# Kernel optimization log

Measured on AMD Instinct MI355X. Metric: run time of the kernel, lower is better.

## Reference

```python
import jax, jax.numpy as jnp
import numpy as np

N, B, L = 1000, 16, 12
H, IN_DIM, OUT_DIM, E = 64, 3, 1, 16000


def _gru_cell(x, h, Wi, Wh, bi, bh):
    # torch nn.GRU gate order: r, z, n
    gi = x @ Wi.T + bi
    gh = h @ Wh.T + bh
    ir, iz, inn = jnp.split(gi, 3, axis=-1)
    hr, hz, hn = jnp.split(gh, 3, axis=-1)
    r = jax.nn.sigmoid(ir + hr)
    z = jax.nn.sigmoid(iz + hz)
    n = jnp.tanh(inn + r * hn)
    return (1.0 - z) * n + z * h


def setup_inputs():
    key = jax.random.key(0)
    ks = jax.random.split(key, 24)
    def rn(k, shape, s=0.1):
        return jax.random.normal(k, shape, dtype=jnp.float32) * s
    return {
        "hidden0": rn(ks[0], (N, B, H), 1.0),
        "hidden1": rn(ks[1], (N, B, H), 1.0),
        "features": rn(ks[2], (N, H), 1.0),
        "labels": rn(ks[3], (N, B, L, IN_DIM), 1.0),
        "edge_index": jax.random.randint(ks[4], (2, E), 0, N),
        # GRU1: input_dim -> H
        "Wi1": rn(ks[5], (3 * H, IN_DIM)), "Wh1": rn(ks[6], (3 * H, H)),
        "bi1": rn(ks[7], (3 * H,)), "bh1": rn(ks[8], (3 * H,)),
        # MetaGAT MLP: 2H -> 16 -> 2 -> 2H*H
        "W1": rn(ks[9], (16, 2 * H)), "b1": rn(ks[10], (16,)),
        "W2": rn(ks[11], (2, 16)), "b2": rn(ks[12], (2,)),
        "W3": rn(ks[13], (2 * H * H, 2)), "b3": rn(ks[14], (2 * H * H,)),
        # GRU2: H -> H
        "Wi2": rn(ks[15], (3 * H, H)), "Wh2": rn(ks[16], (3 * H, H)),
        "bi2": rn(ks[17], (3 * H,)), "bh2": rn(ks[18], (3 * H,)),
        # output layer: 2H -> OUT_DIM
        "Wo": rn(ks[19], (OUT_DIM, 2 * H)), "bo": rn(ks[20], (OUT_DIM,)),
    }


def reference(hidden0, hidden1, features, labels, edge_index,
              Wi1, Wh1, bi1, bh1, W1, b1, W2, b2, W3, b3,
              Wi2, Wh2, bi2, bh2, Wo, bo):
    n, b, length, _ = labels.shape
    h = Wh1.shape[1]
    out_dim = Wo.shape[0]
    in_dim = Wi1.shape[1]
    aux = labels[..., out_dim:]  # [N,B,L,aux_dim]
    # add self loops (as in MetaGAT.forward)
    loops = jnp.arange(n)
    src = jnp.concatenate([edge_index[0], loops])  # j, source
    dst = jnp.concatenate([edge_index[1], loops])  # i, target
    # per-edge weight matrices; features are constant across timesteps so hoist
    ft = jnp.concatenate([features[dst], features[src]], axis=-1)  # [Etot,2H]
    w = jax.nn.sigmoid(ft @ W1.T + b1)
    w = jax.nn.sigmoid(w @ W2.T + b2)
    w = (w @ W3.T + b3).reshape(-1, 2 * h, h)  # [Etot,2H,H]
    feat_b = jnp.broadcast_to(features[:, None, :], (n, b, features.shape[-1]))

    def step(carry, idx):
        h0, h1, prev = carry
        aux_prev = jnp.take(aux, jnp.maximum(idx - 1, 0), axis=2)  # [N,B,aux]
        # eval path (train_mode=False): feed back previous prediction
        data = jnp.where(idx == 0,
                         jnp.zeros((n, b, in_dim), labels.dtype),
                         jnp.concatenate([prev, aux_prev], axis=-1))
        h0n = _gru_cell(data.reshape(n * b, in_dim), h0.reshape(n * b, h),
                        Wi1, Wh1, bi1, bh1).reshape(n, b, h)
        # MetaGAT message passing
        st_j = h0n[src]                                  # [Etot,B,H]
        st = jnp.concatenate([h0n[dst], st_j], axis=-1)  # [Etot,B,2H]
        alpha = jax.nn.leaky_relu(jnp.einsum('ebk,ekh->ebh', st, w), 0.01)
        alpha = jax.nn.softmax(alpha, axis=1)            # softmax over batch dim (faithful to source)
        agg = jax.ops.segment_sum(alpha * st_j, dst, num_segments=n)
        gat = jax.nn.relu(agg)                           # [N,B,H]
        h1n = _gru_cell(gat.reshape(n * b, h), h1.reshape(n * b, h),
                        Wi2, Wh2, bi2, bh2).reshape(n, b, h)
        pred = jnp.concatenate([h1n, feat_b], axis=-1) @ Wo.T + bo  # [N,B,out_dim]
        return (h0n, h1n, pred), pred

    init = (hidden0, hidden1, jnp.zeros((n, b, out_dim), labels.dtype))
    _, preds = jax.lax.scan(step, init, jnp.arange(length))
    return jnp.moveaxis(preds, 0, 2)  # [N,B,L,out_dim]
```

## Files before the change

### kernel.cpp

```cpp
#include <hip/hip_runtime.h>

#define N_NODES 1000
#define BATCH 16
#define SEQ 12
#define IN_DIM 3
#define HDIM 64
#define E_EDGES 16000
#define EN (E_EDGES + N_NODES)
#define NB (N_NODES * BATCH)

typedef unsigned int u32;
typedef unsigned short u16;

__device__ __forceinline__ float sigmoidf(float x) { return 1.0f / (1.0f + expf(-x)); }

__device__ __forceinline__ u16 f2bf(float x) {
    u32 u = __builtin_bit_cast(u32, x);
    u32 r = (u + 0x7fffu + ((u >> 16) & 1u)) >> 16;
    return (u16)r;
}
__device__ __forceinline__ float bf2f(u32 h) {
    return __builtin_bit_cast(float, (h & 0xffffu) << 16);
}
__device__ __forceinline__ u32 pack2(float a, float b) {
    return (u32)f2bf(a) | ((u32)f2bf(b) << 16);
}

__global__ void prep_kernel(const float* __restrict__ hidden0,
                            const float* __restrict__ hidden1,
                            const float* __restrict__ features,
                            const float* __restrict__ W3,
                            const float* __restrict__ b3,
                            const float* __restrict__ Wo,
                            const float* __restrict__ bo,
                            const float* __restrict__ Wh1,
                            const float* __restrict__ Wi1,
                            const float* __restrict__ Wi2,
                            const float* __restrict__ Wh2,
                            float* __restrict__ h0, float* __restrict__ h1,
                            u32* __restrict__ WhPair,
                            u32* __restrict__ Mpair,
                            u32* __restrict__ W2pair,
                            float* __restrict__ Wi1T,
                            float* __restrict__ fpred)
{
    int tid = blockIdx.x * blockDim.x + threadIdx.x;
    int stride = gridDim.x * blockDim.x;

    for (int i = tid; i < NB * HDIM; i += stride) { h0[i] = hidden0[i]; h1[i] = hidden1[i]; }

    for (int i = tid; i < 32 * 192; i += stride) {
        int k2 = i / 192, rem = i % 192;
        int row = rem;
        WhPair[i] = pack2(Wh1[row * 64 + 2 * k2], Wh1[row * 64 + 2 * k2 + 1]);
    }

    for (int i = tid; i < 32 * 384; i += stride) {
        int k2 = i / 384, rem = i % 384;
        int c = rem / 64, h = rem % 64;
        int sel = c % 3;
        float v0, v1;
        {
            int k = 2 * k2;
            int kk = (c < 3 ? k : 64 + k) * 64 + h;
            v0 = (sel == 0) ? W3[kk * 2] : (sel == 1) ? W3[kk * 2 + 1] : b3[kk];
        }
        {
            int k = 2 * k2 + 1;
            int kk = (c < 3 ? k : 64 + k) * 64 + h;
            v1 = (sel == 0) ? W3[kk * 2] : (sel == 1) ? W3[kk * 2 + 1] : b3[kk];
        }
        Mpair[i] = pack2(v0, v1);
    }

    for (int i = tid; i < 32 * 384; i += stride) {
        int k2 = i / 384, rem = i % 384;
        int c = rem / 64, j = rem % 64;
        float v0, v1;
        if (c < 3) {
            int row = c * 64 + j;
            v0 = Wi2[row * 64 + 2 * k2]; v1 = Wi2[row * 64 + 2 * k2 + 1];
        } else {
            int row = (c - 3) * 64 + j;
            v0 = Wh2[row * 64 + 2 * k2]; v1 = Wh2[row * 64 + 2 * k2 + 1];
        }
        W2pair[i] = pack2(v0, v1);
    }

    for (int i = tid; i < 3 * 192; i += stride) {
        int c = i / 192, gj = i % 192;
        Wi1T[i] = Wi1[gj * 3 + c];
    }

    for (int n = tid; n < N_NODES; n += stride) {
        float acc = bo[0];
        for (int h = 0; h < HDIM; ++h) acc += features[n * HDIM + h] * Wo[64 + h];
        fpred[n] = acc;
    }
}

__global__ void deg_init_kernel(int* __restrict__ deg)
{
    int n = blockIdx.x * blockDim.x + threadIdx.x;
    if (n < N_NODES) deg[n] = 1;
}

__global__ void deg_count_kernel(const int* __restrict__ edge_index, int* __restrict__ deg)
{
    int e = blockIdx.x * blockDim.x + threadIdx.x;
    if (e < E_EDGES) atomicAdd(&deg[edge_index[E_EDGES + e]], 1);
}

__global__ __launch_bounds__(1024) void scan_kernel(const int* __restrict__ deg,
                                                    int* __restrict__ row_ptr,
                                                    int* __restrict__ row_fill)
{
    __shared__ int s[1024];
    int tid = threadIdx.x;
    int x = (tid < N_NODES) ? deg[tid] : 0;
    s[tid] = x;
    __syncthreads();
    for (int off = 1; off < 1024; off <<= 1) {
        int v = (tid >= off) ? s[tid - off] : 0;
        __syncthreads();
        s[tid] += v;
        __syncthreads();
    }
    int incl = s[tid];
    int excl = incl - x;
    if (tid < N_NODES) { row_ptr[tid] = excl; row_fill[tid] = excl; }
    if (tid == N_NODES - 1) row_ptr[N_NODES] = incl;
}

__global__ void scatter_kernel(const int* __restrict__ edge_index,
                               int* __restrict__ row_fill,
                               int* __restrict__ csr_src,
                               int* __restrict__ perm)
{
    int e = blockIdx.x * blockDim.x + threadIdx.x;
    if (e < E_EDGES) {
        int s = edge_index[e];
        int d = edge_index[E_EDGES + e];
        int p = atomicAdd(&row_fill[d], 1);
        csr_src[p] = s;
        perm[e] = p;
    } else if (e < EN) {
        int n = e - E_EDGES;
        int p = atomicAdd(&row_fill[n], 1);
        csr_src[p] = n;
        perm[e] = p;
    }
}

__global__ __launch_bounds__(256) void edge_mlp_kernel(const int* __restrict__ edge_index,
                                                       const float* __restrict__ features,
                                                       const float* __restrict__ W1,
                                                       const float* __restrict__ b1,
                                                       const float* __restrict__ W2,
                                                       const float* __restrict__ b2,
                                                       const int* __restrict__ perm,
                                                       float* __restrict__ csr_uv)
{
    int w = threadIdx.x >> 6, j = threadIdx.x & 63;
    int e = blockIdx.x * 4 + w;
    int s, d;
    if (e < E_EDGES) { s = edge_index[e]; d = edge_index[E_EDGES + e]; }
    else             { s = e - E_EDGES; d = s; }

    __shared__ float ft[4][128];
    __shared__ float w1s[4][16];
    ft[w][j]      = features[d * HDIM + j];
    ft[w][64 + j] = features[s * HDIM + j];
    __syncthreads();

    int o = j & 15, part = j >> 4;
    float acc = 0.0f;
    #pragma unroll 8
    for (int kk = 0; kk < 32; ++kk)
        acc += ft[w][part * 32 + kk] * W1[o * 128 + part * 32 + kk];
    acc += __shfl_xor(acc, 16, 64);
    acc += __shfl_xor(acc, 32, 64);
    if (j < 16) w1s[w][j] = sigmoidf(acc + b1[j]);
    __syncthreads();
    if (j < 2) {
        float a2 = b2[j];
        #pragma unroll
        for (int k = 0; k < 16; ++k) a2 += w1s[w][k] * W2[j * 16 + k];
        csr_uv[perm[e] * 2 + j] = sigmoidf(a2);
    }
}

__global__ __launch_bounds__(512) void gru1_proj_kernel(const float* __restrict__ labels,
                                                        const float* __restrict__ prev,
                                                        const float* __restrict__ Wi1T,
                                                        const u32* __restrict__ WhPair,
                                                        const float* __restrict__ bi1,
                                                        const float* __restrict__ bh1,
                                                        const u32* __restrict__ Mpair,
                                                        float* __restrict__ h0,
                                                        uint2* __restrict__ Pd,
                                                        uint2* __restrict__ Ps,
                                                        int t)
{
    int tid = threadIdx.x;
    int w = tid >> 6, j = tid & 63;
    int rbase = blockIdx.x * 64 + w * 8;

    __shared__ u32 sWh[32 * 192];
    __shared__ u32 sM[32 * 384];
    __shared__ float hs[64][64];

    for (int i = tid; i < 32 * 192; i += 512) sWh[i] = WhPair[i];
    for (int i = tid; i < 32 * 384; i += 512) sM[i] = Mpair[i];
    #pragma unroll
    for (int rr = 0; rr < 8; ++rr)
        hs[w * 8 + rr][j] = h0[(size_t)(rbase + rr) * HDIM + j];
    __syncthreads();

    float ar[8], az[8], an[8];
    {
        float br = bh1[j], bz = bh1[64 + j], bn = bh1[128 + j];
        #pragma unroll
        for (int rr = 0; rr < 8; ++rr) { ar[rr] = br; az[rr] = bz; an[rr] = bn; }
    }

    for (int k2 = 0; k2 < 32; ++k2) {
        u32 pr = sWh[k2 * 192 + j];
        u32 pz = sWh[k2 * 192 + 64 + j];
        u32 pn = sWh[k2 * 192 + 128 + j];
        float wr0 = bf2f(pr), wr1 = bf2f(pr >> 16);
        float wz0 = bf2f(pz), wz1 = bf2f(pz >> 16);
        float wn0 = bf2f(pn), wn1 = bf2f(pn >> 16);
        #pragma unroll
        for (int rr = 0; rr < 8; ++rr) {
            float2 h2 = *(const float2*)&hs[w * 8 + rr][2 * k2];
            ar[rr] = fmaf(wr0, h2.x, ar[rr]); ar[rr] = fmaf(wr1, h2.y, ar[rr]);
            az[rr] = fmaf(wz0, h2.x, az[rr]); az[rr] = fmaf(wz1, h2.y, az[rr]);
            an[rr] = fmaf(wn0, h2.x, an[rr]); an[rr] = fmaf(wn1, h2.y, an[rr]);
        }
    }

    float wi00 = Wi1T[j],       wi01 = Wi1T[64 + j],       wi02 = Wi1T[128 + j];
    float wi10 = Wi1T[192 + j], wi11 = Wi1T[192 + 64 + j], wi12 = Wi1T[192 + 128 + j];
    float wi20 = Wi1T[384 + j], wi21 = Wi1T[384 + 64 + j], wi22 = Wi1T[384 + 128 + j];
    float bir = bi1[j], biz = bi1[64 + j], bin_ = bi1[128 + j];

    #pragma unroll
    for (int rr = 0; rr < 8; ++rr) {
        int row = rbase + rr;
        float x0 = 0.f, x1 = 0.f, x2 = 0.f;
        if (t > 0) {
            x0 = prev[row];
            const float* lab = labels + ((size_t)row * SEQ + (t - 1)) * IN_DIM;
            x1 = lab[1]; x2 = lab[2];
        }
        float gir = bir  + x0 * wi00 + x1 * wi10 + x2 * wi20;
        float giz = biz  + x0 * wi01 + x1 * wi11 + x2 * wi21;
        float gin = bin_ + x0 * wi02 + x1 * wi12 + x2 * wi22;
        float rg = sigmoidf(gir + ar[rr]);
        float zg = sigmoidf(giz + az[rr]);
        float ng = tanhf(gin + rg * an[rr]);
        float hj = hs[w * 8 + rr][j];
        float hn = (1.0f - zg) * ng + zg * hj;
        h0[(size_t)row * HDIM + j] = hn;
        hs[w * 8 + rr][j] = hn;
    }

    float a0[8], a1[8], a2[8], a3[8], a4[8], a5[8];
    #pragma unroll
    for (int rr = 0; rr < 8; ++rr) { a0[rr]=0.f; a1[rr]=0.f; a2[rr]=0.f; a3[rr]=0.f; a4[rr]=0.f; a5[rr]=0.f; }

    for (int k2 = 0; k2 < 32; ++k2) {
        u32 p0 = sM[k2 * 384 + j];
        u32 p1 = sM[k2 * 384 + 64 + j];
        u32 p2 = sM[k2 * 384 + 128 + j];
        u32 p3 = sM[k2 * 384 + 192 + j];
        u32 p4 = sM[k2 * 384 + 256 + j];
        u32 p5 = sM[k2 * 384 + 320 + j];
        float m00 = bf2f(p0), m01 = bf2f(p0 >> 16);
        float m10 = bf2f(p1), m11 = bf2f(p1 >> 16);
        float m20 = bf2f(p2), m21 = bf2f(p2 >> 16);
        float m30 = bf2f(p3), m31 = bf2f(p3 >> 16);
        float m40 = bf2f(p4), m41 = bf2f(p4 >> 16);
        float m50 = bf2f(p5), m51 = bf2f(p5 >> 16);
        #pragma unroll
        for (int rr = 0; rr < 8; ++rr) {
            float2 h2 = *(const float2*)&hs[w * 8 + rr][2 * k2];
            a0[rr] = fmaf(m00, h2.x, a0[rr]); a0[rr] = fmaf(m01, h2.y, a0[rr]);
            a1[rr] = fmaf(m10, h2.x, a1[rr]); a1[rr] = fmaf(m11, h2.y, a1[rr]);
            a2[rr] = fmaf(m20, h2.x, a2[rr]); a2[rr] = fmaf(m21, h2.y, a2[rr]);
            a3[rr] = fmaf(m30, h2.x, a3[rr]); a3[rr] = fmaf(m31, h2.y, a3[rr]);
            a4[rr] = fmaf(m40, h2.x, a4[rr]); a4[rr] = fmaf(m41, h2.y, a4[rr]);
            a5[rr] = fmaf(m50, h2.x, a5[rr]); a5[rr] = fmaf(m51, h2.y, a5[rr]);
        }
    }

    #pragma unroll
    for (int rr = 0; rr < 8; ++rr) {
        size_t row = rbase + rr;
        float stj = hs[w * 8 + rr][j];
        Pd[row * 64 + j] = make_uint2(pack2(a0[rr], a1[rr]), pack2(a2[rr], 0.f));
        Ps[row * 64 + j] = make_uint2(pack2(a3[rr], a4[rr]), pack2(a5[rr], stj));
    }
}

__global__ __launch_bounds__(256) void edge_step_kernel(const int* __restrict__ row_ptr,
                                                        const int* __restrict__ csr_src,
                                                        const float* __restrict__ csr_uv,
                                                        const uint2* __restrict__ Pd,
                                                        const uint2* __restrict__ Ps,
                                                        float* __restrict__ agg)
{
    int d = blockIdx.x;
    int w = threadIdx.x >> 6, h = threadIdx.x & 63;

    uint2 pdreg[BATCH];
    #pragma unroll
    for (int b = 0; b < BATCH; ++b)
        pdreg[b] = Pd[((size_t)d * BATCH + b) * 64 + h];

    float acc[BATCH];
    #pragma unroll
    for (int b = 0; b < BATCH; ++b) acc[b] = 0.0f;

    int start = row_ptr[d], end = row_ptr[d + 1];
    for (int p = start + w; p < end; p += 4) {
        int s = csr_src[p];
        float u = csr_uv[p * 2], v = csr_uv[p * 2 + 1];

        float al[BATCH], stj[BATCH];
        #pragma unroll
        for (int b = 0; b < BATCH; ++b) {
            uint2 pd = pdreg[b];
            uint2 ps = Ps[((size_t)s * BATCH + b) * 64 + h];
            float a = u * (bf2f(pd.x) + bf2f(ps.x))
                    + v * (bf2f(pd.x >> 16) + bf2f(ps.x >> 16))
                    + bf2f(pd.y) + bf2f(ps.y);
            al[b] = (a > 0.0f) ? a : 0.01f * a;
            stj[b] = bf2f(ps.y >> 16);
        }
        float m = al[0];
        #pragma unroll
        for (int b = 1; b < BATCH; ++b) m = fmaxf(m, al[b]);
        float sum = 0.0f;
        #pragma unroll
        for (int b = 0; b < BATCH; ++b) { al[b] = expf(al[b] - m); sum += al[b]; }
        float inv = 1.0f / sum;
        #pragma unroll
        for (int b = 0; b < BATCH; ++b) acc[b] = fmaf(al[b] * inv, stj[b], acc[b]);
    }

    __shared__ float red[4][BATCH][HDIM];
    #pragma unroll
    for (int b = 0; b < BATCH; ++b) red[w][b][h] = acc[b];
    __syncthreads();

    for (int c = threadIdx.x; c < BATCH * HDIM; c += 256) {
        float s4 = red[0][0][c] + red[1][0][c] + red[2][0][c] + red[3][0][c];
        agg[(size_t)d * BATCH * HDIM + c] = s4;
    }
}

__global__ __launch_bounds__(512) void gru2_pred_kernel(const float* __restrict__ agg,
                                                        const u32* __restrict__ W2pair,
                                                        const float* __restrict__ bi2,
                                                        const float* __restrict__ bh2,
                                                        const float* __restrict__ Wo,
                                                        const float* __restrict__ fpred,
                                                        float* __restrict__ h1,
                                                        float* __restrict__ prev,
                                                        float* __restrict__ out,
                                                        int t)
{
    int tid = threadIdx.x;
    int w = tid >> 6, j = tid & 63;
    int rbase = blockIdx.x * 64 + w * 8;

    __shared__ u32 sW2[32 * 384];
    __shared__ float gs[64][64];
    __shared__ float hs[64][64];

    for (int i = tid; i < 32 * 384; i += 512) sW2[i] = W2pair[i];
    #pragma unroll
    for (int rr = 0; rr < 8; ++rr) {
        float g = agg[(size_t)(rbase + rr) * HDIM + j];
        gs[w * 8 + rr][j] = fmaxf(g, 0.0f);
        hs[w * 8 + rr][j] = h1[(size_t)(rbase + rr) * HDIM + j];
    }
    __syncthreads();

    float acr[8], acz[8], ain[8], ahn[8];
    {
        float b0 = bi2[j] + bh2[j], b1 = bi2[64 + j] + bh2[64 + j];
        float b2 = bi2[128 + j], c2 = bh2[128 + j];
        #pragma unroll
        for (int rr = 0; rr < 8; ++rr) { acr[rr] = b0; acz[rr] = b1; ain[rr] = b2; ahn[rr] = c2; }
    }

    for (int k2 = 0; k2 < 32; ++k2) {
        u32 pir = sW2[k2 * 384 + j];
        u32 piz = sW2[k2 * 384 + 64 + j];
        u32 pin = sW2[k2 * 384 + 128 + j];
        u32 phr = sW2[k2 * 384 + 192 + j];
        u32 phz = sW2[k2 * 384 + 256 + j];
        u32 phn = sW2[k2 * 384 + 320 + j];
        float wir0 = bf2f(pir), wir1 = bf2f(pir >> 16);
        float wiz0 = bf2f(piz), wiz1 = bf2f(piz >> 16);
        float win0 = bf2f(pin), win1 = bf2f(pin >> 16);
        float whr0 = bf2f(phr), whr1 = bf2f(phr >> 16);
        float whz0 = bf2f(phz), whz1 = bf2f(phz >> 16);
        float whn0 = bf2f(phn), whn1 = bf2f(phn >> 16);
        #pragma unroll
        for (int rr = 0; rr < 8; ++rr) {
            float2 g2 = *(const float2*)&gs[w * 8 + rr][2 * k2];
            float2 h2 = *(const float2*)&hs[w * 8 + rr][2 * k2];
            acr[rr] = fmaf(wir0, g2.x, acr[rr]); acr[rr] = fmaf(wir1, g2.y, acr[rr]);
            acr[rr] = fmaf(whr0, h2.x, acr[rr]); acr[rr] = fmaf(whr1, h2.y, acr[rr]);
            acz[rr] = fmaf(wiz0, g2.x, acz[rr]); acz[rr] = fmaf(wiz1, g2.y, acz[rr]);
            acz[rr] = fmaf(whz0, h2.x, acz[rr]); acz[rr] = fmaf(whz1, h2.y, acz[rr]);
            ain[rr] = fmaf(win0, g2.x, ain[rr]); ain[rr] = fmaf(win1, g2.y, ain[rr]);
            ahn[rr] = fmaf(whn0, h2.x, ahn[rr]); ahn[rr] = fmaf(whn1, h2.y, ahn[rr]);
        }
    }

    float woj = Wo[j];
    #pragma unroll
    for (int rr = 0; rr < 8; ++rr) {
        float rg = sigmoidf(acr[rr]);
        float zg = sigmoidf(acz[rr]);
        float ng = tanhf(ain[rr] + rg * ahn[rr]);
        float hj = hs[w * 8 + rr][j];
        float hn = (1.0f - zg) * ng + zg * hj;
        h1[(size_t)(rbase + rr) * HDIM + j] = hn;

        float part = hn * woj;
        #pragma unroll
        for (int off = 32; off; off >>= 1) part += __shfl_xor(part, off, 64);
        if (j == rr) {
            int row = rbase + rr;
            float p = part + fpred[row / BATCH];
            prev[row] = p;
            out[(size_t)row * SEQ + t] = p;
        }
    }
}

extern "C" void kernel_launch(void* const* d_in, const int* in_sizes, int n_in,
                              void* d_out, int out_size, void* d_ws, size_t ws_size,
                              hipStream_t stream)
{
    const float* hidden0  = (const float*)d_in[0];
    const float* hidden1  = (const float*)d_in[1];
    const float* features = (const float*)d_in[2];
    const float* labels   = (const float*)d_in[3];
    const int*   edge_idx = (const int*)d_in[4];
    const float* Wi1 = (const float*)d_in[5];
    const float* Wh1 = (const float*)d_in[6];
    const float* bi1 = (const float*)d_in[7];
    const float* bh1 = (const float*)d_in[8];
    const float* W1  = (const float*)d_in[9];
    const float* b1  = (const float*)d_in[10];
    const float* W2  = (const float*)d_in[11];
    const float* b2  = (const float*)d_in[12];
    const float* W3  = (const float*)d_in[13];
    const float* b3  = (const float*)d_in[14];
    const float* Wi2 = (const float*)d_in[15];
    const float* Wh2 = (const float*)d_in[16];
    const float* bi2 = (const float*)d_in[17];
    const float* bh2 = (const float*)d_in[18];
    const float* Wo  = (const float*)d_in[19];
    const float* bo  = (const float*)d_in[20];

    float* ws = (float*)d_ws;
    float* h0    = ws;  ws += NB * HDIM;
    float* h1    = ws;  ws += NB * HDIM;
    uint2* Pd    = (uint2*)ws;  ws += NB * HDIM * 2;
    uint2* Ps    = (uint2*)ws;  ws += NB * HDIM * 2;
    float* agg   = ws;  ws += NB * HDIM;
    float* csr_uv= ws;  ws += EN * 2;
    u32*   WhPair = (u32*)ws;  ws += 32 * 192;
    u32*   Mpair  = (u32*)ws;  ws += 32 * 384;
    u32*   W2pair = (u32*)ws;  ws += 32 * 384;
    float* Wi1T  = ws;  ws += 3 * 192;
    float* fpred = ws;  ws += N_NODES;
    float* prev  = ws;  ws += NB;
    int*   deg      = (int*)ws;  ws += N_NODES;
    int*   row_ptr  = (int*)ws;  ws += N_NODES + 1;
    int*   row_fill = (int*)ws;  ws += N_NODES;
    int*   csr_src  = (int*)ws;  ws += EN;
    int*   perm     = (int*)ws;  ws += EN;
    float* out   = (float*)d_out;

    prep_kernel<<<256, 256, 0, stream>>>(hidden0, hidden1, features, W3, b3, Wo, bo,
                                         Wh1, Wi1, Wi2, Wh2,
                                         h0, h1, WhPair, Mpair, W2pair, Wi1T, fpred);
    deg_init_kernel<<<(N_NODES + 255) / 256, 256, 0, stream>>>(deg);
    deg_count_kernel<<<(E_EDGES + 255) / 256, 256, 0, stream>>>(edge_idx, deg);
    scan_kernel<<<1, 1024, 0, stream>>>(deg, row_ptr, row_fill);
    scatter_kernel<<<(EN + 255) / 256, 256, 0, stream>>>(edge_idx, row_fill, csr_src, perm);
    edge_mlp_kernel<<<(EN + 3) / 4, 256, 0, stream>>>(edge_idx, features, W1, b1, W2, b2,
                                                      perm, csr_uv);

    for (int t = 0; t < SEQ; ++t) {
        gru1_proj_kernel<<<NB / 64, 512, 0, stream>>>(labels, prev, Wi1T, WhPair, bi1, bh1,
                                                      Mpair, h0, Pd, Ps, t);
        edge_step_kernel<<<N_NODES, 256, 0, stream>>>(row_ptr, csr_src, csr_uv, Pd, Ps, agg);
        gru2_pred_kernel<<<NB / 64, 512, 0, stream>>>(agg, W2pair, bi2, bh2, Wo, fpred,
                                                      h1, prev, out, t);
    }
}
```

Measured before the change: 1.045 ms.

## Replace per-timestep kernel triplet with a persistent cooperative kernel using grid sync

The 36 per-timestep launches are replaced by one cooperative kernel with one block per node. Each block keeps its node's GRU hidden states in shared memory across all timesteps and uses a grid-wide sync only before the edge aggregation. The source projections are double-buffered so the next step's writes never overwrite data another block is still reading. This removes launch overhead and global round-trips for h0, h1, Pd and agg, at the cost of grid-sync latency and a lower-occupancy fused kernel. The old path is kept as a fallback if the cooperative launch fails.

Result: slower. 2.606 ms (+149.3%).

```diff
diff --git a/kernel.cpp b/kernel.cpp
--- a/kernel.cpp
+++ b/kernel.cpp
@@ -1,4 +1,7 @@
 #include <hip/hip_runtime.h>
+#include <hip/hip_cooperative_groups.h>
+
+namespace cg = cooperative_groups;
 
 #define N_NODES 1000
 #define BATCH 16
@@ -50,8 +53,7 @@
     for (int i = tid; i < NB * HDIM; i += stride) { h0[i] = hidden0[i]; h1[i] = hidden1[i]; }
 
     for (int i = tid; i < 32 * 192; i += stride) {
-        int k2 = i / 192, rem = i % 192;
-        int row = rem;
+        int k2 = i / 192, row = i % 192;
         WhPair[i] = pack2(Wh1[row * 64 + 2 * k2], Wh1[row * 64 + 2 * k2 + 1]);
     }
 
@@ -187,6 +189,243 @@
         #pragma unroll
         for (int k = 0; k < 16; ++k) a2 += w1s[w][k] * W2[j * 16 + k];
         csr_uv[perm[e] * 2 + j] = sigmoidf(a2);
+    }
+}
+
+__global__ __launch_bounds__(256, 4) void persist_kernel(
+    const float* __restrict__ hidden0,
+    const float* __restrict__ hidden1,
+    const float* __restrict__ labels,
+    const int* __restrict__ row_ptr,
+    const int* __restrict__ csr_src,
+    const float* __restrict__ csr_uv,
+    const float* __restrict__ Wi1T,
+    const u32* __restrict__ WhPair,
+    const float* __restrict__ bi1,
+    const float* __restrict__ bh1,
+    const u32* __restrict__ Mpair,
+    const u32* __restrict__ W2pair,
+    const float* __restrict__ bi2,
+    const float* __restrict__ bh2,
+    const float* __restrict__ Wo,
+    const float* __restrict__ fpred,
+    uint2* __restrict__ PsA,
+    uint2* __restrict__ PsB,
+    float* __restrict__ out)
+{
+    cg::grid_group grid = cg::this_grid();
+
+    int d = blockIdx.x;
+    int tid = threadIdx.x;
+    int w = tid >> 6, j = tid & 63;
+    int rb = w * 4;
+    int growbase = d * BATCH;
+
+    __shared__ float hs0[BATCH][HDIM];
+    __shared__ float hs1[BATCH][HDIM];
+    __shared__ float gs[BATCH][HDIM];
+    __shared__ float red[4][BATCH][HDIM];
+    __shared__ uint2 sPd[BATCH][HDIM];
+    __shared__ float prevs[BATCH];
+
+    #pragma unroll
+    for (int rr = 0; rr < 4; ++rr) {
+        hs0[rb + rr][j] = hidden0[(size_t)(growbase + rb + rr) * HDIM + j];
+        hs1[rb + rr][j] = hidden1[(size_t)(growbase + rb + rr) * HDIM + j];
+    }
+    int start = row_ptr[d], end = row_ptr[d + 1];
+
+    for (int t = 0; t < SEQ; ++t) {
+        uint2* PsCur = (t & 1) ? PsB : PsA;
+
+        {
+            float bhr = bh1[j], bhz = bh1[64 + j], bhn = bh1[128 + j];
+            float ar[4], az[4], an[4];
+            #pragma unroll
+            for (int rr = 0; rr < 4; ++rr) { ar[rr] = bhr; az[rr] = bhz; an[rr] = bhn; }
+
+            for (int k2 = 0; k2 < 32; ++k2) {
+                u32 pr = WhPair[k2 * 192 + j];
+                u32 pz = WhPair[k2 * 192 + 64 + j];
+                u32 pn = WhPair[k2 * 192 + 128 + j];
+                float wr0 = bf2f(pr), wr1 = bf2f(pr >> 16);
+                float wz0 = bf2f(pz), wz1 = bf2f(pz >> 16);
+                float wn0 = bf2f(pn), wn1 = bf2f(pn >> 16);
+                #pragma unroll
+                for (int rr = 0; rr < 4; ++rr) {
+                    float2 h2 = *(const float2*)&hs0[rb + rr][2 * k2];
+                    ar[rr] = fmaf(wr0, h2.x, ar[rr]); ar[rr] = fmaf(wr1, h2.y, ar[rr]);
+                    az[rr] = fmaf(wz0, h2.x, az[rr]); az[rr] = fmaf(wz1, h2.y, az[rr]);
+                    an[rr] = fmaf(wn0, h2.x, an[rr]); an[rr] = fmaf(wn1, h2.y, an[rr]);
+                }
+            }
+
+            float wi00 = Wi1T[j],       wi01 = Wi1T[64 + j],       wi02 = Wi1T[128 + j];
+            float wi10 = Wi1T[192 + j], wi11 = Wi1T[192 + 64 + j], wi12 = Wi1T[192 + 128 + j];
+            float wi20 = Wi1T[384 + j], wi21 = Wi1T[384 + 64 + j], wi22 = Wi1T[384 + 128 + j];
+            float bir = bi1[j], biz = bi1[64 + j], bin_ = bi1[128 + j];
+
+            #pragma unroll
+            for (int rr = 0; rr < 4; ++rr) {
+                int lrow = rb + rr;
+                float x0 = 0.f, x1 = 0.f, x2 = 0.f;
+                if (t > 0) {
+                    x0 = prevs[lrow];
+                    const float* lab = labels + ((size_t)(growbase + lrow) * SEQ + (t - 1)) * IN_DIM;
+                    x1 = lab[1]; x2 = lab[2];
+                }
+                float gir = bir  + x0 * wi00 + x1 * wi10 + x2 * wi20;
+                float giz = biz  + x0 * wi01 + x1 * wi11 + x2 * wi21;
+                float gin = bin_ + x0 * wi02 + x1 * wi12 + x2 * wi22;
+                float rg = sigmoidf(gir + ar[rr]);
+                float zg = sigmoidf(giz + az[rr]);
+                float ng = tanhf(gin + rg * an[rr]);
+                float hj = hs0[lrow][j];
+                hs0[lrow][j] = (1.0f - zg) * ng + zg * hj;
+            }
+        }
+
+        {
+            float a0[4], a1[4], a2[4], a3[4], a4[4], a5[4];
+            #pragma unroll
+            for (int rr = 0; rr < 4; ++rr) { a0[rr]=0.f; a1[rr]=0.f; a2[rr]=0.f; a3[rr]=0.f; a4[rr]=0.f; a5[rr]=0.f; }
+
+            for (int k2 = 0; k2 < 32; ++k2) {
+                u32 p0 = Mpair[k2 * 384 + j];
+                u32 p1 = Mpair[k2 * 384 + 64 + j];
+                u32 p2 = Mpair[k2 * 384 + 128 + j];
+                u32 p3 = Mpair[k2 * 384 + 192 + j];
+                u32 p4 = Mpair[k2 * 384 + 256 + j];
+                u32 p5 = Mpair[k2 * 384 + 320 + j];
+                float m00 = bf2f(p0), m01 = bf2f(p0 >> 16);
+                float m10 = bf2f(p1), m11 = bf2f(p1 >> 16);
+                float m20 = bf2f(p2), m21 = bf2f(p2 >> 16);
+                float m30 = bf2f(p3), m31 = bf2f(p3 >> 16);
+                float m40 = bf2f(p4), m41 = bf2f(p4 >> 16);
+                float m50 = bf2f(p5), m51 = bf2f(p5 >> 16);
+                #pragma unroll
+                for (int rr = 0; rr < 4; ++rr) {
+                    float2 h2 = *(const float2*)&hs0[rb + rr][2 * k2];
+                    a0[rr] = fmaf(m00, h2.x, a0[rr]); a0[rr] = fmaf(m01, h2.y, a0[rr]);
+                    a1[rr] = fmaf(m10, h2.x, a1[rr]); a1[rr] = fmaf(m11, h2.y, a1[rr]);
+                    a2[rr] = fmaf(m20, h2.x, a2[rr]); a2[rr] = fmaf(m21, h2.y, a2[rr]);
+                    a3[rr] = fmaf(m30, h2.x, a3[rr]); a3[rr] = fmaf(m31, h2.y, a3[rr]);
+                    a4[rr] = fmaf(m40, h2.x, a4[rr]); a4[rr] = fmaf(m41, h2.y, a4[rr]);
+                    a5[rr] = fmaf(m50, h2.x, a5[rr]); a5[rr] = fmaf(m51, h2.y, a5[rr]);
+                }
+            }
+
+            #pragma unroll
+            for (int rr = 0; rr < 4; ++rr) {
+                int lrow = rb + rr;
+                float stj = hs0[lrow][j];
+                sPd[lrow][j] = make_uint2(pack2(a0[rr], a1[rr]), pack2(a2[rr], 0.f));
+                PsCur[((size_t)(growbase + lrow)) * 64 + j] =
+                    make_uint2(pack2(a3[rr], a4[rr]), pack2(a5[rr], stj));
+            }
+        }
+
+        grid.sync();
+
+        {
+            float acc[BATCH];
+            #pragma unroll
+            for (int b = 0; b < BATCH; ++b) acc[b] = 0.0f;
+
+            const uint2* PsIn = (t & 1) ? PsB : PsA;
+            for (int p = start + w; p < end; p += 4) {
+                int s = csr_src[p];
+                float u = csr_uv[2 * p], v = csr_uv[2 * p + 1];
+                const uint2* psrow = PsIn + ((size_t)s * BATCH) * 64 + j;
+
+                float al[BATCH], stj[BATCH];
+                #pragma unroll
+                for (int b = 0; b < BATCH; ++b) {
+                    uint2 pd = sPd[b][j];
+                    uint2 ps = psrow[(size_t)b * 64];
+                    float a = u * (bf2f(pd.x) + bf2f(ps.x))
+                            + v * (bf2f(pd.x >> 16) + bf2f(ps.x >> 16))
+                            + bf2f(pd.y) + bf2f(ps.y);
+                    al[b] = (a > 0.0f) ? a : 0.01f * a;
+                    stj[b] = bf2f(ps.y >> 16);
+                }
+                float m = al[0];
+                #pragma unroll
+                for (int b = 1; b < BATCH; ++b) m = fmaxf(m, al[b]);
+                float sum = 0.0f;
+                #pragma unroll
+                for (int b = 0; b < BATCH; ++b) { al[b] = expf(al[b] - m); sum += al[b]; }
+                float inv = 1.0f / sum;
+                #pragma unroll
+                for (int b = 0; b < BATCH; ++b) acc[b] = fmaf(al[b] * inv, stj[b], acc[b]);
+            }
+
+            #pragma unroll
+            for (int b = 0; b < BATCH; ++b) red[w][b][j] = acc[b];
+            __syncthreads();
+            for (int c = tid; c < BATCH * HDIM; c += 256) {
+                float s4 = red[0][0][c] + red[1][0][c] + red[2][0][c] + red[3][0][c];
+                gs[0][c] = fmaxf(s4, 0.0f);
+            }
+            __syncthreads();
+        }
+
+        {
+            float b2r = bi2[j] + bh2[j];
+            float b2z = bi2[64 + j] + bh2[64 + j];
+            float b2in = bi2[128 + j], b2hn = bh2[128 + j];
+            float acr[4], acz[4], ain2[4], ahn2[4];
+            #pragma unroll
+            for (int rr = 0; rr < 4; ++rr) { acr[rr] = b2r; acz[rr] = b2z; ain2[rr] = b2in; ahn2[rr] = b2hn; }
+
+            for (int k2 = 0; k2 < 32; ++k2) {
+                u32 pir = W2pair[k2 * 384 + j];
+                u32 piz = W2pair[k2 * 384 + 64 + j];
+                u32 pin = W2pair[k2 * 384 + 128 + j];
+                u32 phr = W2pair[k2 * 384 + 192 + j];
+                u32 phz = W2pair[k2 * 384 + 256 + j];
+                u32 phn = W2pair[k2 * 384 + 320 + j];
+                float wir0 = bf2f(pir), wir1 = bf2f(pir >> 16);
+                float wiz0 = bf2f(piz), wiz1 = bf2f(piz >> 16);
+                float win0 = bf2f(pin), win1 = bf2f(pin >> 16);
+                float whr0 = bf2f(phr), whr1 = bf2f(phr >> 16);
+                float whz0 = bf2f(phz), whz1 = bf2f(phz >> 16);
+                float whn0 = bf2f(phn), whn1 = bf2f(phn >> 16);
+                #pragma unroll
+                for (int rr = 0; rr < 4; ++rr) {
+                    float2 g2 = *(const float2*)&gs[rb + rr][2 * k2];
+                    float2 h2 = *(const float2*)&hs1[rb + rr][2 * k2];
+                    acr[rr] = fmaf(wir0, g2.x, acr[rr]); acr[rr] = fmaf(wir1, g2.y, acr[rr]);
+                    acr[rr] = fmaf(whr0, h2.x, acr[rr]); acr[rr] = fmaf(whr1, h2.y, acr[rr]);
+                    acz[rr] = fmaf(wiz0, g2.x, acz[rr]); acz[rr] = fmaf(wiz1, g2.y, acz[rr]);
+                    acz[rr] = fmaf(whz0, h2.x, acz[rr]); acz[rr] = fmaf(whz1, h2.y, acz[rr]);
+                    ain2[rr] = fmaf(win0, g2.x, ain2[rr]); ain2[rr] = fmaf(win1, g2.y, ain2[rr]);
+                    ahn2[rr] = fmaf(whn0, h2.x, ahn2[rr]); ahn2[rr] = fmaf(whn1, h2.y, ahn2[rr]);
+                }
+            }
+
+            float woj = Wo[j];
+            float fp = fpred[d];
+            #pragma unroll
+            for (int rr = 0; rr < 4; ++rr) {
+                int lrow = rb + rr;
+                float rg = sigmoidf(acr[rr]);
+                float zg = sigmoidf(acz[rr]);
+                float ng = tanhf(ain2[rr] + rg * ahn2[rr]);
+                float hj = hs1[lrow][j];
+                float hn = (1.0f - zg) * ng + zg * hj;
+                hs1[lrow][j] = hn;
+
+                float part = hn * woj;
+                #pragma unroll
+                for (int off = 32; off; off >>= 1) part += __shfl_xor(part, off, 64);
+                if (j == rr) {
+                    float p = part + fp;
+                    prevs[lrow] = p;
+                    out[(size_t)(growbase + lrow) * SEQ + t] = p;
+                }
+            }
+        }
     }
 }
 
@@ -476,6 +715,8 @@
     float* h1    = ws;  ws += NB * HDIM;
     uint2* Pd    = (uint2*)ws;  ws += NB * HDIM * 2;
     uint2* Ps    = (uint2*)ws;  ws += NB * HDIM * 2;
+    uint2* PsA   = (uint2*)ws;  ws += NB * HDIM * 2;
+    uint2* PsB   = (uint2*)ws;  ws += NB * HDIM * 2;
     float* agg   = ws;  ws += NB * HDIM;
     float* csr_uv= ws;  ws += EN * 2;
     u32*   WhPair = (u32*)ws;  ws += 32 * 192;
@@ -501,11 +742,33 @@
     edge_mlp_kernel<<<(EN + 3) / 4, 256, 0, stream>>>(edge_idx, features, W1, b1, W2, b2,
                                                       perm, csr_uv);
 
-    for (int t = 0; t < SEQ; ++t) {
-        gru1_proj_kernel<<<NB / 64, 512, 0, stream>>>(labels, prev, Wi1T, WhPair, bi1, bh1,
-                                                      Mpair, h0, Pd, Ps, t);
-        edge_step_kernel<<<N_NODES, 256, 0, stream>>>(row_ptr, csr_src, csr_uv, Pd, Ps, agg);
-        gru2_pred_kernel<<<NB / 64, 512, 0, stream>>>(agg, W2pair, bi2, bh2, Wo, fpred,
-                                                      h1, prev, out, t);
-    }
-}
+    const int* row_ptr_c = row_ptr;
+    const int* csr_src_c = csr_src;
+    const float* csr_uv_c = csr_uv;
+    const float* Wi1T_c = Wi1T;
+    const u32* WhPair_c = WhPair;
+    const u32* Mpair_c = Mpair;
+    const u32* W2pair_c = W2pair;
+    const float* fpred_c = fpred;
+    void* args[] = {
+        (void*)&hidden0, (void*)&hidden1, (void*)&labels,
+        (void*)&row_ptr_c, (void*)&csr_src_c, (void*)&csr_uv_c,
+        (void*)&Wi1T_c, (void*)&WhPair_c, (void*)&bi1, (void*)&bh1,
+        (void*)&Mpair_c, (void*)&W2pair_c, (void*)&bi2, (void*)&bh2,
+        (void*)&Wo, (void*)&fpred_c, (void*)&PsA, (void*)&PsB, (void*)&out
+    };
+    hipError_t cerr = hipLaunchCooperativeKernel((void*)persist_kernel,
+                                                 dim3(N_NODES), dim3(256),
+                                                 args, 0, stream);
+    if (cerr != hipSuccess) {
+        (void)hipGetLastError();
+        for (int t = 0; t < SEQ; ++t) {
+            gru1_proj_kernel<<<NB / 64, 512, 0, stream>>>(labels, prev, Wi1T, WhPair,
+                                                          bi1, bh1, Mpair, h0, Pd, Ps, t);
+            edge_step_kernel<<<N_NODES, 256, 0, stream>>>(row_ptr, csr_src, csr_uv,
+                                                          Pd, Ps, agg);
+            gru2_pred_kernel<<<NB / 64, 512, 0, stream>>>(agg, W2pair, bi2, bh2, Wo, fpred,
+                                                          h1, prev, out, t);
+        }
+    }
+}
```
